# Kernel optimization log

Measured on AMD Instinct MI355X. Metric: run time of the kernel, lower is better.

Reference implementation:

```python
import jax, jax.numpy as jnp
import numpy as np

K = 5          # kernel_size per dim
B = 100        # batch size (hard-coded in source)
GRID = 28
NUM_FIRST_FC = 49  # adjs[2].size(0) = 7*7


def spline_conv(x, edge_index, pseudo, W, root, bias):
    """Degree-1 open B-spline graph conv (SplineGCN).
    x: [N, Cin]; edge_index: [2, E] (src, dst); pseudo: [E, 2] in [0,1];
    W: [K*K, Cin, Cout]; root: [Cin, Cout]; bias: [Cout].
    out_i = mean_{j->i} sum_taps b_tap(u_ij) * (x_j @ W[k_tap]) + x_i @ root + bias
    """
    N = x.shape[0]
    src, dst = edge_index[0], edge_index[1]
    pos = pseudo * (K - 1)                     # open spline: scale to [0, K-1]
    kf = jnp.floor(pos)
    frac = pos - kf                            # [E, 2]
    k0 = kf.astype(jnp.int32)
    k1 = jnp.minimum(k0 + 1, K - 1)
    # Precompute x @ W[k] for all 25 kernel indices: [N, K*K, Cout]
    y = jnp.einsum('ni,kio->nko', x, W)
    fx, fy = frac[:, 0], frac[:, 1]
    taps = [
        (k0[:, 0], k0[:, 1], (1 - fx) * (1 - fy)),
        (k0[:, 0], k1[:, 1], (1 - fx) * fy),
        (k1[:, 0], k0[:, 1], fx * (1 - fy)),
        (k1[:, 0], k1[:, 1], fx * fy),
    ]
    msg = jnp.zeros((src.shape[0], W.shape[2]), dtype=x.dtype)
    for ax, ay, w in taps:
        msg = msg + w[:, None] * y[src, ax * K + ay]   # gather [E, Cout]
    agg = jax.ops.segment_sum(msg, dst, num_segments=N)
    deg = jax.ops.segment_sum(jnp.ones_like(msg[:, 0]), dst, num_segments=N)
    return agg / jnp.maximum(deg, 1.0)[:, None] + x @ root + bias


def max_pool2(x):  # x: [b, H, W, C] -> [b, H/2, W/2, C] (same math as NCHW pool)
    b, h, w, c = x.shape
    return x.reshape(b, h // 2, 2, w // 2, 2, c).max(axis=(2, 4))


def setup_inputs() -> dict:
    key = jax.random.key(0)
    ks = jax.random.split(key, 16)
    N0, N1 = B * GRID * GRID, B * (GRID // 2) * (GRID // 2)
    E0, E1 = N0 * 8, N1 * 8
    s = 0.1
    return {
        'x': jax.random.normal(ks[0], (N0, 1), dtype=jnp.float32),
        'pseudo0': jax.random.uniform(ks[1], (E0, 2), dtype=jnp.float32),
        'pseudo1': jax.random.uniform(ks[2], (E1, 2), dtype=jnp.float32),
        'W1': jax.random.normal(ks[3], (K * K, 1, 32), dtype=jnp.float32) * s,
        'root1': jax.random.normal(ks[4], (1, 32), dtype=jnp.float32) * s,
        'b1': jnp.zeros((32,), dtype=jnp.float32),
        'W2': jax.random.normal(ks[5], (K * K, 32, 64), dtype=jnp.float32) * s,
        'root2': jax.random.normal(ks[6], (32, 64), dtype=jnp.float32) * s,
        'b2': jnp.zeros((64,), dtype=jnp.float32),
        'fc1_w': jax.random.normal(ks[7], (NUM_FIRST_FC * 64, 512), dtype=jnp.float32) * 0.02,
        'fc1_b': jnp.zeros((512,), dtype=jnp.float32),
        'fc2_w': jax.random.normal(ks[8], (512, 10), dtype=jnp.float32) * 0.02,
        'fc2_b': jnp.zeros((10,), dtype=jnp.float32),
        'edge_index0': jax.random.randint(ks[9], (2, E0), 0, N0, dtype=jnp.int32),
        'edge_index1': jax.random.randint(ks[10], (2, E1), 0, N1, dtype=jnp.int32),
    }


def reference(x, pseudo0, pseudo1, W1, root1, b1, W2, root2, b2,
              fc1_w, fc1_b, fc2_w, fc2_b, edge_index0, edge_index1):
    elu = jax.nn.elu
    # conv1 on 28x28 grid graph
    h = elu(spline_conv(x, edge_index0, pseudo0, W1, root1, b1))   # [B*784, 32]
    h = h.reshape(-1, GRID, GRID, 32)                              # [B, 28, 28, 32]
    h = max_pool2(h)                                               # [B, 14, 14, 32]
    h = h.reshape(-1, 32)                                          # [B*196, 32]
    # conv2 on 14x14 grid graph
    h = elu(spline_conv(h, edge_index1, pseudo1, W2, root2, b2))   # [B*196, 64]
    # faithful replication of the source's reshapes: (B*196) rows -> (B/4, 28, 28, 64)
    h = h.reshape(-1, GRID, GRID, 64)                              # [25, 28, 28, 64]
    h = max_pool2(h)                                               # [25, 14, 14, 64]
    h = h.reshape(-1, NUM_FIRST_FC * 64)                           # [100, 3136]
    h = elu(h @ fc1_w + fc1_b)
    # F.dropout with training=False (eval) is identity
    h = elu(h @ fc2_w + fc2_b)
    return jax.nn.log_softmax(h, axis=-1)
```

## Files before the change

kernel.cpp:

```cpp
#include <hip/hip_runtime.h>
#include <hip/hip_bf16.h>

#define KK 5
constexpr int N0 = 78400;
constexpr int E0 = 627200;
constexpr int N1 = 19600;
constexpr int E1 = 156800;
constexpr int C1 = 32, C2 = 64;
constexpr int BSZ = 100;
constexpr int FC1_IN = 3136, FC1_OUT = 512;
constexpr int KEXT = 832;
constexpr int ULS = 836;
constexpr int UBS = 856;
constexpr int KZ = 7;

constexpr int NB0 = 1400;
constexpr int CAP0 = 576;
constexpr int NB1 = 1225;
constexpr int CAP1 = 224;
constexpr int NBT = NB0 + NB1;

constexpr float SC1  = 4194304.f;
constexpr float ISC1 = 1.f / 4194304.f;
constexpr float SC2  = 1048576.f;
constexpr float ISC2 = 1.f / 1048576.f;

typedef __attribute__((ext_vector_type(8))) short bf16x8;
typedef __attribute__((ext_vector_type(4))) float f32x4;

__device__ __forceinline__ unsigned short f2bf(float f) {
    union { float f; unsigned u; } v; v.f = f;
    unsigned u = v.u;
    unsigned r = (u + 0x7FFF + ((u >> 16) & 1)) >> 16;
    return (unsigned short)r;
}
__device__ __forceinline__ float bf2f(unsigned short h) {
    return __uint_as_float(((unsigned)h) << 16);
}

__device__ __forceinline__ unsigned fenc(float f) {
    unsigned u = __float_as_uint(f);
    return (u & 0x80000000u) ? ~u : (u | 0x80000000u);
}
__device__ __forceinline__ unsigned short fdec_bf(unsigned e) {
    unsigned u = (e & 0x80000000u) ? (e & 0x7FFFFFFFu) : ~e;
    return f2bf(__uint_as_float(u));
}

__device__ __forceinline__ void taps4(float px, float py,
                                      int& a00, int& a01, int& a10, int& a11,
                                      float& fx, float& fy) {
    float kfx = floorf(px), kfy = floorf(py);
    fx = px - kfx; fy = py - kfy;
    int k0x = min(max((int)kfx, 0), KK - 1);
    int k0y = min(max((int)kfy, 0), KK - 1);
    int k1x = min(k0x + 1, KK - 1), k1y = min(k0y + 1, KK - 1);
    a00 = k0x * KK + k0y; a01 = k0x * KK + k1y;
    a10 = k1x * KK + k0y; a11 = k1x * KK + k1y;
}

__global__ void coarse_bin(const int* __restrict__ ei0, const int* __restrict__ ei1,
                           const float* __restrict__ ps0, const float* __restrict__ ps1,
                           int* __restrict__ gcur,
                           int2* __restrict__ pk0, int2* __restrict__ pk1,
                           const float* __restrict__ fc1w, const float* __restrict__ W2,
                           const float* __restrict__ root2,
                           unsigned short* __restrict__ wt1,
                           unsigned short* __restrict__ w2t,
                           unsigned* __restrict__ pmax) {
    __shared__ int hist[NBT];
    __shared__ int gbase[NBT];
    __shared__ unsigned short tile[64 * 66];
    int t = threadIdx.x;
    if (blockIdx.x >= 192) {
        int pb = blockIdx.x - 192;
        if (pb >= 400) {
            for (int idx = (pb - 400) * 512 + t; idx < 112 * FC1_IN; idx += 8 * 512)
                pmax[idx] = (idx < 100 * FC1_IN) ? 0x007FFFFFu
                                                 : 0x80000000u;
            return;
        }
        if (pb >= 392) {
            int base = (pb - 392) * 6656;
            for (int i2 = t; i2 < 6656; i2 += 512) {
                int idx = base + i2;
                int o = idx / KEXT, k = idx - o * KEXT;
                float v = (k < 800) ? W2[k * 64 + o] : root2[(k - 800) * 64 + o];
                w2t[idx] = f2bf(v);
            }
            return;
        }
        int k0 = (pb >> 3) * 64, j0 = (pb & 7) * 64;
        int jj = t & 63, ks = t >> 6;
        for (int kk = ks; kk < 64; kk += 8)
            tile[kk * 66 + jj] = f2bf(fc1w[(k0 + kk) * FC1_OUT + j0 + jj]);
        __syncthreads();
        int kk2 = t & 63, js = t >> 6;
        for (int j2 = js; j2 < 64; j2 += 8)
            wt1[(j0 + j2) * FC1_IN + k0 + kk2] = tile[kk2 * 66 + j2];
        return;
    }
    for (int i = t; i < NBT; i += 512) hist[i] = 0;
    __syncthreads();
    int e0b = blockIdx.x * 4096;
    int keys[8], rnk[8], pay0[8], pay1[8];
#pragma unroll
    for (int j = 0; j < 8; j++) {
        int e = e0b + t + j * 512;
        int k = -1, p0 = 0, p1v = 0;
        if (e < E0) {
            int dst = ei0[E0 + e];
            int b = dst / 56, low = dst - b * 56;
            k = b;
            float px = ps0[2 * e] * 4.f, py = ps0[2 * e + 1] * 4.f;
            unsigned ux = min((unsigned)(px * 16384.f + 0.5f), 65535u);
            unsigned uy = min((unsigned)(py * 16384.f + 0.5f), 65535u);
            p0 = ei0[e] | (low << 20); p1v = (int)(ux | (uy << 16));
        } else if (e < E0 + E1) {
            int el = e - E0;
            int dst = ei1[E1 + el];
            k = NB0 + (dst >> 4);
            float px = ps1[2 * el] * 4.f, py = ps1[2 * el + 1] * 4.f;
            unsigned ux = min((unsigned)(px * 16384.f + 0.5f), 65535u);
            unsigned uy = min((unsigned)(py * 16384.f + 0.5f), 65535u);
            p0 = ei1[el] | ((dst & 15) << 20); p1v = (int)(ux | (uy << 16));
        }
        keys[j] = k; pay0[j] = p0; pay1[j] = p1v;
    }
#pragma unroll
    for (int j = 0; j < 8; j++)
        if (keys[j] >= 0) rnk[j] = atomicAdd(&hist[keys[j]], 1);
    __syncthreads();
    for (int i = t; i < NBT; i += 512)
        gbase[i] = hist[i] ? atomicAdd(&gcur[i], hist[i]) : 0;
    __syncthreads();
#pragma unroll
    for (int j = 0; j < 8; j++) {
        if (keys[j] >= 0) {
            int k = keys[j];
            int p = gbase[k] + rnk[j];
            if (k < NB0) {
                if (p < CAP0) pk0[k * CAP0 + p] = make_int2(pay0[j], pay1[j]);
            } else {
                if (p < CAP1) pk1[(k - NB0) * CAP1 + p] = make_int2(pay0[j], pay1[j]);
            }
        }
    }
}

__global__ __launch_bounds__(256, 6)
void conv1_pool(const int2* __restrict__ pk0, const int* __restrict__ cnt0,
                const float* __restrict__ x,
                const float* __restrict__ W1,
                const float* __restrict__ root, const float* __restrict__ bias,
                unsigned short* __restrict__ p1b) {
    __shared__ int   Ui[56 * 26];
    __shared__ float h1t[56 * 32];
    int t = threadIdx.x;
    int bb = blockIdx.x;
    int n0 = bb * 56;
    for (int i = t; i < 56 * 26; i += 256) Ui[i] = 0;
    __syncthreads();
    int cnt = min(cnt0[bb], CAP0);
    const int2* bkt = pk0 + bb * CAP0;
    for (int j = t; j < cnt; j += 256) {
        int2 r = bkt[j];
        int src = r.x & 0xFFFFF, low = (r.x >> 20) & 63;
        float px = (float)((unsigned)r.y & 0xFFFF) * (1.f / 16384.f);
        float py = (float)((unsigned)r.y >> 16) * (1.f / 16384.f);
        int a00, a01, a10, a11; float fx, fy;
        taps4(px, py, a00, a01, a10, a11, fx, fy);
        float xv = x[src];
        float gx = 1.f - fx, gy = 1.f - fy;
        int* row = Ui + low * 26;
        atomicAdd(row + a00, __float2int_rn(gx * gy * xv * SC1));
        atomicAdd(row + a01, __float2int_rn(gx * fy * xv * SC1));
        atomicAdd(row + a10, __float2int_rn(fx * gy * xv * SC1));
        atomicAdd(row + a11, __float2int_rn(fx * fy * xv * SC1));
        atomicAdd(row + 25, 1);
    }
    __syncthreads();
    {
        int o = t & 31, ng = t >> 5;
        float w1c[25];
#pragma unroll
        for (int a = 0; a < 25; a++) w1c[a] = W1[a * C1 + o];
        float ro = root[o], bo = bias[o];
        for (int j2 = 0; j2 < 7; j2++) {
            int nl = ng * 7 + j2;
            int n = n0 + nl;
            float acc = 0.f;
#pragma unroll
            for (int a = 0; a < 25; a++) acc += (float)Ui[nl * 26 + a] * w1c[a];
            float invd = ISC1 / fmaxf((float)Ui[nl * 26 + 25], 1.f);
            float v = acc * invd + x[n] * ro + bo;
            h1t[nl * 32 + o] = v > 0.f ? v : expm1f(v);
        }
    }
    __syncthreads();
    for (int i2 = t; i2 < 448; i2 += 256) {
        int o2 = i2 & 31, pc = i2 >> 5;
        float m0 = h1t[(2 * pc) * 32 + o2],      m1 = h1t[(2 * pc + 1) * 32 + o2];
        float m2 = h1t[(28 + 2 * pc) * 32 + o2], m3 = h1t[(28 + 2 * pc + 1) * 32 + o2];
        p1b[(bb * 14 + pc) * C1 + o2] = f2bf(fmaxf(fmaxf(m0, m1), fmaxf(m2, m3)));
    }
}

__global__ __launch_bounds__(512, 2)
void conv2_fused(const unsigned short* __restrict__ p1b, const int2* __restrict__ pk1,
                 const int* __restrict__ cnt1,
                 const unsigned short* __restrict__ w2t,
                 const float* __restrict__ b2, unsigned* __restrict__ pmax) {
    __shared__ int   Ui[16 * ULS];
    __shared__ int   es[CAP1];
    __shared__ int   et[CAP1];
    __shared__ float efx[CAP1], efy[CAP1];
    __shared__ int   degc[16];
    unsigned short* Ub = (unsigned short*)Ui;
    int t = threadIdx.x;
    int bx = blockIdx.x;
    int nb = bx * 16;
    int i = t & 31;
    int g = t >> 5;
    int* up = Ui + g * ULS;
#pragma unroll
    for (int a = 0; a < 25; a++) up[a * 32 + i] = 0;
    up[800 + i] = __float2int_rn(bf2f(p1b[(nb + g) * C1 + i]) * SC2);
    if (t < 16) degc[t] = 0;
    __syncthreads();
    int cnt = min(cnt1[bx], CAP1);
    for (int j = t; j < cnt; j += 512) {
        int2 r = pk1[bx * CAP1 + j];
        es[j] = r.x;
        float px = (float)((unsigned)r.y & 0xFFFF) * (1.f / 16384.f);
        float py = (float)((unsigned)r.y >> 16) * (1.f / 16384.f);
        int a00, a01, a10, a11; float fx, fy;
        taps4(px, py, a00, a01, a10, a11, fx, fy);
        et[j] = a00 | (a01 << 5) | (a10 << 10) | (a11 << 15);
        efx[j] = fx; efy[j] = fy;
        atomicAdd(&degc[(r.x >> 20) & 15], 1);
    }
    __syncthreads();
    for (int j = g; j < cnt; j += 16) {
        int rx = es[j];
        float xv = bf2f(p1b[(rx & 0xFFFFF) * C1 + i]);
        int* row = Ui + ((rx >> 20) & 15) * ULS;
        int m = et[j];
        float fx = efx[j], fy = efy[j];
        float gx = 1.f - fx, gy = 1.f - fy;
        atomicAdd(row + (m & 31) * 32 + i,         __float2int_rn(gx * gy * xv * SC2));
        atomicAdd(row + ((m >> 5) & 31) * 32 + i,  __float2int_rn(gx * fy * xv * SC2));
        atomicAdd(row + ((m >> 10) & 31) * 32 + i, __float2int_rn(fx * gy * xv * SC2));
        atomicAdd(row + ((m >> 15) & 31) * 32 + i, __float2int_rn(fx * fy * xv * SC2));
    }
    __syncthreads();
    {
        int g2 = t >> 5, i2c = t & 31;
        float invd = 1.f / fmaxf((float)degc[g2], 1.f);
        float stap = ISC2 * invd;
        const int* srcp = Ui + g2 * ULS + i2c * 26;
        float rv[26];
#pragma unroll
        for (int j = 0; j < 26; j++) {
            float v = (float)srcp[j];
            rv[j] = (i2c * 26 + j < 800) ? v * stap : v * ISC2;
        }
        __syncthreads();
        unsigned* dstp = (unsigned*)(Ub + g2 * UBS + i2c * 26);
#pragma unroll
        for (int j = 0; j < 13; j++) {
            unsigned lo = f2bf(rv[2 * j]), hi = f2bf(rv[2 * j + 1]);
            dstp[j] = lo | (hi << 16);
        }
    }
    __syncthreads();
    int wv = t >> 6, lane = t & 63, quad = lane >> 4, lrow = lane & 15;
    if (wv < 4) {
        f32x4 acc = {0.f, 0.f, 0.f, 0.f};
        const unsigned short* bbase = w2t + (wv * 16 + lrow) * KEXT;
        const unsigned short* abase = Ub + lrow * UBS;
#pragma unroll
        for (int kc = 0; kc < 26; kc++) {
            bf16x8 a = *(const bf16x8*)(abase + kc * 32 + quad * 8);
            bf16x8 b = *(const bf16x8*)(bbase + kc * 32 + quad * 8);
            acc = __builtin_amdgcn_mfma_f32_16x16x32_bf16(a, b, acc, 0, 0, 0);
        }
        int o = wv * 16 + lrow;
        float bo = b2[o];
#pragma unroll
        for (int r = 0; r < 4; r++) {
            int node = quad * 4 + r;
            float v = acc[r] + bo;
            v = v > 0.f ? v : expm1f(v);
            int n1 = nb + node;
            int b28 = n1 / 784;
            int rem = n1 - b28 * 784;
            int rr = rem / 28, cc = rem - rr * 28;
            int flat = ((b28 * 14 + (rr >> 1)) * 14 + (cc >> 1)) * 64 + o;
            atomicMax(&pmax[flat], fenc(v));
        }
    }
}

__global__ void gemm_fc1(const unsigned* __restrict__ pmax,
                         const unsigned short* __restrict__ wt1,
                         float* __restrict__ z1p) {
    constexpr int AS = 232;
    __shared__ unsigned short as_[16 * AS];
    int t = threadIdx.x;
    int jt = blockIdx.x, mt = blockIdx.y, kz = blockIdx.z;
    int wv = t >> 6, lane = t & 63, quad = lane >> 4, lrow = lane & 15;
    int m0 = mt * 16;
    int kbase = kz * 448;
    const unsigned short* bbase = wt1 + (jt * 64 + wv * 16 + lrow) * FC1_IN + kbase;
    f32x4 acc = {0.f, 0.f, 0.f, 0.f};
    for (int ch = 0; ch < 2; ch++) {
        __syncthreads();
        for (int slot = t; slot < 448; slot += 256) {
            int r = slot / 28, c = slot - (slot / 28) * 28;
            const unsigned* gp = pmax + (m0 + r) * FC1_IN + kbase + ch * 224 + c * 8;
            uint4 e0 = *(const uint4*)gp;
            uint4 e1 = *(const uint4*)(gp + 4);
            unsigned w0 = (unsigned)fdec_bf(e0.x) | ((unsigned)fdec_bf(e0.y) << 16);
            unsigned w1 = (unsigned)fdec_bf(e0.z) | ((unsigned)fdec_bf(e0.w) << 16);
            unsigned w2 = (unsigned)fdec_bf(e1.x) | ((unsigned)fdec_bf(e1.y) << 16);
            unsigned w3 = (unsigned)fdec_bf(e1.z) | ((unsigned)fdec_bf(e1.w) << 16);
            *(uint4*)(as_ + r * AS + c * 8) = make_uint4(w0, w1, w2, w3);
        }
        __syncthreads();
        const unsigned short* ab = as_ + lrow * AS;
        const unsigned short* bb = bbase + ch * 224;
#pragma unroll
        for (int kk = 0; kk < 7; kk++) {
            bf16x8 a = *(const bf16x8*)(ab + kk * 32 + quad * 8);
            bf16x8 b = *(const bf16x8*)(bb + kk * 32 + quad * 8);
            acc = __builtin_amdgcn_mfma_f32_16x16x32_bf16(a, b, acc, 0, 0, 0);
        }
    }
    int n = jt * 64 + wv * 16 + lrow;
#pragma unroll
    for (int r = 0; r < 4; r++) {
        int m = m0 + quad * 4 + r;
        z1p[kz * (112 * FC1_OUT) + m * FC1_OUT + n] = acc[r];
    }
}

__global__ void fc2_lsm(const float* __restrict__ z1p, const float* __restrict__ fc1b,
                        const float* __restrict__ w, const float* __restrict__ fc2b,
                        float* __restrict__ out) {
    int b = blockIdx.x;
    int t = threadIdx.x;
    int wv = t >> 6;
    int lane = t & 63;
    float acc = 0.f;
#pragma unroll
    for (int m = 0; m < 8; m++) {
        int k = lane * 8 + m;
        float xv = fc1b[k];
#pragma unroll
        for (int p = 0; p < KZ; p++)
            xv += z1p[p * (112 * FC1_OUT) + b * FC1_OUT + k];
        xv = xv > 0.f ? xv : expm1f(xv);
        acc += xv * w[k * 10 + wv];
    }
#pragma unroll
    for (int off = 32; off > 0; off >>= 1) acc += __shfl_down(acc, off);
    __shared__ float zs[10];
    if (lane == 0) {
        float z = acc + fc2b[wv];
        zs[wv] = z > 0.f ? z : expm1f(z);
    }
    __syncthreads();
    if (t < 10) {
        float m = -1e30f;
        for (int jj = 0; jj < 10; jj++) m = fmaxf(m, zs[jj]);
        float s = 0.f;
        for (int jj = 0; jj < 10; jj++) s += expf(zs[jj] - m);
        out[b * 10 + t] = zs[t] - m - logf(s);
    }
}

extern "C" void kernel_launch(void* const* d_in, const int* in_sizes, int n_in,
                              void* d_out, int out_size, void* d_ws, size_t ws_size,
                              hipStream_t stream) {
    const float* x     = (const float*)d_in[0];
    const float* ps0   = (const float*)d_in[1];
    const float* ps1   = (const float*)d_in[2];
    const float* W1    = (const float*)d_in[3];
    const float* root1 = (const float*)d_in[4];
    const float* b1    = (const float*)d_in[5];
    const float* W2    = (const float*)d_in[6];
    const float* root2 = (const float*)d_in[7];
    const float* b2v   = (const float*)d_in[8];
    const float* fc1w  = (const float*)d_in[9];
    const float* fc1b  = (const float*)d_in[10];
    const float* fc2w  = (const float*)d_in[11];
    const float* fc2b  = (const float*)d_in[12];
    const int*   ei0   = (const int*)d_in[13];
    const int*   ei1   = (const int*)d_in[14];

    float* ws = (float*)d_ws;
    int*  gcur = (int*)ws;
    int2* pk0  = (int2*)(ws + 2688);
    int2* pk1  = (int2*)(ws + 1615488);
    unsigned short* p1b = (unsigned short*)(ws + 2164288);
    unsigned* pmax = (unsigned*)(ws + 2477888);
    float* z1p = ws + 2829120;
    unsigned short* w2t = (unsigned short*)(ws + 3230528);
    unsigned short* wt1 = (unsigned short*)(ws + 3257152);

    hipMemsetAsync(gcur, 0, (size_t)NBT * sizeof(int), stream);

    coarse_bin<<<600, 512, 0, stream>>>(ei0, ei1, ps0, ps1, gcur, pk0, pk1,
                                        fc1w, W2, root2, wt1, w2t, pmax);
    conv1_pool<<<NB0, 256, 0, stream>>>(pk0, gcur, x, W1, root1, b1, p1b);
    conv2_fused<<<NB1, 512, 0, stream>>>(p1b, pk1, gcur + NB0, w2t, b2v, pmax);
    gemm_fc1<<<dim3(8, 7, KZ), 256, 0, stream>>>(pmax, wt1, z1p);
    fc2_lsm<<<BSZ, 640, 0, stream>>>(z1p, fc1b, fc2w, fc2b, (float*)d_out);
}
```

Before: 185.2 us.

## Fuse conv1, conv2, fc1 and fc2 into one persistent cooperative kernel

Replaces four separate kernel launches with a single persistent cooperative kernel that loops over the former block indices and separates stages with grid-wide syncs. This removes the launch gaps and tail effects between stages. In exchange, each stage runs with at most 1024 resident blocks of 512 threads, conv1 switches from 256 to 512 threads per work item with idle threads, and the grid barriers themselves add cost. Shared memory is sized for the largest stage, which may lower occupancy for the conv1 phase.

```diff
diff --git a/kernel.cpp b/kernel.cpp
--- a/kernel.cpp
+++ b/kernel.cpp
@@ -1,5 +1,8 @@
 #include <hip/hip_runtime.h>
 #include <hip/hip_bf16.h>
+#include <hip/hip_cooperative_groups.h>
+
+namespace cg = cooperative_groups;
 
 #define KK 5
 constexpr int N0 = 78400;
@@ -148,235 +151,249 @@
     }
 }
 
-__global__ __launch_bounds__(256, 6)
-void conv1_pool(const int2* __restrict__ pk0, const int* __restrict__ cnt0,
-                const float* __restrict__ x,
-                const float* __restrict__ W1,
-                const float* __restrict__ root, const float* __restrict__ bias,
-                unsigned short* __restrict__ p1b) {
-    __shared__ int   Ui[56 * 26];
-    __shared__ float h1t[56 * 32];
+__global__ __launch_bounds__(512)
+void fused_net(const int2* __restrict__ pk0, const int2* __restrict__ pk1,
+               const int* __restrict__ gcur,
+               const float* __restrict__ x, const float* __restrict__ W1,
+               const float* __restrict__ root1, const float* __restrict__ b1,
+               const unsigned short* __restrict__ w2t, const float* __restrict__ b2,
+               const unsigned short* __restrict__ wt1, const float* __restrict__ fc1b,
+               const float* __restrict__ fc2w, const float* __restrict__ fc2b,
+               unsigned short* __restrict__ p1b, unsigned* __restrict__ pmax,
+               float* __restrict__ z1p, float* __restrict__ out) {
+    cg::grid_group grid = cg::this_grid();
+    __shared__ int UiS[16 * ULS];
+    __shared__ int esS[CAP1];
+    __shared__ int etS[CAP1];
+    __shared__ float efxS[CAP1], efyS[CAP1];
+    __shared__ int degc[16];
     int t = threadIdx.x;
-    int bb = blockIdx.x;
-    int n0 = bb * 56;
-    for (int i = t; i < 56 * 26; i += 256) Ui[i] = 0;
-    __syncthreads();
-    int cnt = min(cnt0[bb], CAP0);
-    const int2* bkt = pk0 + bb * CAP0;
-    for (int j = t; j < cnt; j += 256) {
-        int2 r = bkt[j];
-        int src = r.x & 0xFFFFF, low = (r.x >> 20) & 63;
-        float px = (float)((unsigned)r.y & 0xFFFF) * (1.f / 16384.f);
-        float py = (float)((unsigned)r.y >> 16) * (1.f / 16384.f);
-        int a00, a01, a10, a11; float fx, fy;
-        taps4(px, py, a00, a01, a10, a11, fx, fy);
-        float xv = x[src];
-        float gx = 1.f - fx, gy = 1.f - fy;
-        int* row = Ui + low * 26;
-        atomicAdd(row + a00, __float2int_rn(gx * gy * xv * SC1));
-        atomicAdd(row + a01, __float2int_rn(gx * fy * xv * SC1));
-        atomicAdd(row + a10, __float2int_rn(fx * gy * xv * SC1));
-        atomicAdd(row + a11, __float2int_rn(fx * fy * xv * SC1));
-        atomicAdd(row + 25, 1);
-    }
-    __syncthreads();
+    int i = t & 31, g = t >> 5;
+    int wv = t >> 6, lane = t & 63, quad = lane >> 4, lrow = lane & 15;
+
     {
-        int o = t & 31, ng = t >> 5;
-        float w1c[25];
-#pragma unroll
-        for (int a = 0; a < 25; a++) w1c[a] = W1[a * C1 + o];
-        float ro = root[o], bo = bias[o];
-        for (int j2 = 0; j2 < 7; j2++) {
-            int nl = ng * 7 + j2;
-            int n = n0 + nl;
-            float acc = 0.f;
-#pragma unroll
-            for (int a = 0; a < 25; a++) acc += (float)Ui[nl * 26 + a] * w1c[a];
-            float invd = ISC1 / fmaxf((float)Ui[nl * 26 + 25], 1.f);
-            float v = acc * invd + x[n] * ro + bo;
-            h1t[nl * 32 + o] = v > 0.f ? v : expm1f(v);
-        }
-    }
-    __syncthreads();
-    for (int i2 = t; i2 < 448; i2 += 256) {
-        int o2 = i2 & 31, pc = i2 >> 5;
-        float m0 = h1t[(2 * pc) * 32 + o2],      m1 = h1t[(2 * pc + 1) * 32 + o2];
-        float m2 = h1t[(28 + 2 * pc) * 32 + o2], m3 = h1t[(28 + 2 * pc + 1) * 32 + o2];
-        p1b[(bb * 14 + pc) * C1 + o2] = f2bf(fmaxf(fmaxf(m0, m1), fmaxf(m2, m3)));
-    }
-}
-
-__global__ __launch_bounds__(512, 2)
-void conv2_fused(const unsigned short* __restrict__ p1b, const int2* __restrict__ pk1,
-                 const int* __restrict__ cnt1,
-                 const unsigned short* __restrict__ w2t,
-                 const float* __restrict__ b2, unsigned* __restrict__ pmax) {
-    __shared__ int   Ui[16 * ULS];
-    __shared__ int   es[CAP1];
-    __shared__ int   et[CAP1];
-    __shared__ float efx[CAP1], efy[CAP1];
-    __shared__ int   degc[16];
-    unsigned short* Ub = (unsigned short*)Ui;
-    int t = threadIdx.x;
-    int bx = blockIdx.x;
-    int nb = bx * 16;
-    int i = t & 31;
-    int g = t >> 5;
-    int* up = Ui + g * ULS;
-#pragma unroll
-    for (int a = 0; a < 25; a++) up[a * 32 + i] = 0;
-    up[800 + i] = __float2int_rn(bf2f(p1b[(nb + g) * C1 + i]) * SC2);
-    if (t < 16) degc[t] = 0;
-    __syncthreads();
-    int cnt = min(cnt1[bx], CAP1);
-    for (int j = t; j < cnt; j += 512) {
-        int2 r = pk1[bx * CAP1 + j];
-        es[j] = r.x;
-        float px = (float)((unsigned)r.y & 0xFFFF) * (1.f / 16384.f);
-        float py = (float)((unsigned)r.y >> 16) * (1.f / 16384.f);
-        int a00, a01, a10, a11; float fx, fy;
-        taps4(px, py, a00, a01, a10, a11, fx, fy);
-        et[j] = a00 | (a01 << 5) | (a10 << 10) | (a11 << 15);
-        efx[j] = fx; efy[j] = fy;
-        atomicAdd(&degc[(r.x >> 20) & 15], 1);
-    }
-    __syncthreads();
-    for (int j = g; j < cnt; j += 16) {
-        int rx = es[j];
-        float xv = bf2f(p1b[(rx & 0xFFFFF) * C1 + i]);
-        int* row = Ui + ((rx >> 20) & 15) * ULS;
-        int m = et[j];
-        float fx = efx[j], fy = efy[j];
-        float gx = 1.f - fx, gy = 1.f - fy;
-        atomicAdd(row + (m & 31) * 32 + i,         __float2int_rn(gx * gy * xv * SC2));
-        atomicAdd(row + ((m >> 5) & 31) * 32 + i,  __float2int_rn(gx * fy * xv * SC2));
-        atomicAdd(row + ((m >> 10) & 31) * 32 + i, __float2int_rn(fx * gy * xv * SC2));
-        atomicAdd(row + ((m >> 15) & 31) * 32 + i, __float2int_rn(fx * fy * xv * SC2));
-    }
-    __syncthreads();
+        int* Ui = UiS;
+        float* h1t = (float*)(UiS + 56 * 26);
+        for (int bb = blockIdx.x; bb < NB0; bb += gridDim.x) {
+            int n0 = bb * 56;
+            for (int k = t; k < 56 * 26; k += 512) Ui[k] = 0;
+            __syncthreads();
+            int cnt = min(gcur[bb], CAP0);
+            const int2* bkt = pk0 + bb * CAP0;
+            for (int j = t; j < cnt; j += 512) {
+                int2 r = bkt[j];
+                int src = r.x & 0xFFFFF, low = (r.x >> 20) & 63;
+                float px = (float)((unsigned)r.y & 0xFFFF) * (1.f / 16384.f);
+                float py = (float)((unsigned)r.y >> 16) * (1.f / 16384.f);
+                int a00, a01, a10, a11; float fx, fy;
+                taps4(px, py, a00, a01, a10, a11, fx, fy);
+                float xv = x[src];
+                float gx = 1.f - fx, gy = 1.f - fy;
+                int* row = Ui + low * 26;
+                atomicAdd(row + a00, __float2int_rn(gx * gy * xv * SC1));
+                atomicAdd(row + a01, __float2int_rn(gx * fy * xv * SC1));
+                atomicAdd(row + a10, __float2int_rn(fx * gy * xv * SC1));
+                atomicAdd(row + a11, __float2int_rn(fx * fy * xv * SC1));
+                atomicAdd(row + 25, 1);
+            }
+            __syncthreads();
+            {
+                float w1c[25];
+#pragma unroll
+                for (int a = 0; a < 25; a++) w1c[a] = W1[a * C1 + i];
+                float ro = root1[i], bo = b1[i];
+#pragma unroll
+                for (int j2 = 0; j2 < 4; j2++) {
+                    int nl = g * 4 + j2;
+                    if (nl < 56) {
+                        int n = n0 + nl;
+                        float acc = 0.f;
+#pragma unroll
+                        for (int a = 0; a < 25; a++)
+                            acc += (float)Ui[nl * 26 + a] * w1c[a];
+                        float invd = ISC1 / fmaxf((float)Ui[nl * 26 + 25], 1.f);
+                        float v = acc * invd + x[n] * ro + bo;
+                        h1t[nl * 32 + i] = v > 0.f ? v : expm1f(v);
+                    }
+                }
+            }
+            __syncthreads();
+            for (int i2 = t; i2 < 448; i2 += 512) {
+                int o2 = i2 & 31, pc = i2 >> 5;
+                float m0 = h1t[(2 * pc) * 32 + o2],      m1 = h1t[(2 * pc + 1) * 32 + o2];
+                float m2 = h1t[(28 + 2 * pc) * 32 + o2], m3 = h1t[(28 + 2 * pc + 1) * 32 + o2];
+                p1b[(bb * 14 + pc) * C1 + o2] = f2bf(fmaxf(fmaxf(m0, m1), fmaxf(m2, m3)));
+            }
+            __syncthreads();
+        }
+    }
+    grid.sync();
     {
-        int g2 = t >> 5, i2c = t & 31;
-        float invd = 1.f / fmaxf((float)degc[g2], 1.f);
-        float stap = ISC2 * invd;
-        const int* srcp = Ui + g2 * ULS + i2c * 26;
-        float rv[26];
-#pragma unroll
-        for (int j = 0; j < 26; j++) {
-            float v = (float)srcp[j];
-            rv[j] = (i2c * 26 + j < 800) ? v * stap : v * ISC2;
+        unsigned short* Ub = (unsigned short*)UiS;
+        const int* cnt1 = gcur + NB0;
+        for (int bx = blockIdx.x; bx < NB1; bx += gridDim.x) {
+            int nb = bx * 16;
+            int* up = UiS + g * ULS;
+#pragma unroll
+            for (int a = 0; a < 25; a++) up[a * 32 + i] = 0;
+            up[800 + i] = __float2int_rn(bf2f(p1b[(nb + g) * C1 + i]) * SC2);
+            if (t < 16) degc[t] = 0;
+            __syncthreads();
+            int cnt = min(cnt1[bx], CAP1);
+            for (int j = t; j < cnt; j += 512) {
+                int2 r = pk1[bx * CAP1 + j];
+                esS[j] = r.x;
+                float px = (float)((unsigned)r.y & 0xFFFF) * (1.f / 16384.f);
+                float py = (float)((unsigned)r.y >> 16) * (1.f / 16384.f);
+                int a00, a01, a10, a11; float fx, fy;
+                taps4(px, py, a00, a01, a10, a11, fx, fy);
+                etS[j] = a00 | (a01 << 5) | (a10 << 10) | (a11 << 15);
+                efxS[j] = fx; efyS[j] = fy;
+                atomicAdd(&degc[(r.x >> 20) & 15], 1);
+            }
+            __syncthreads();
+            for (int j = g; j < cnt; j += 16) {
+                int rx = esS[j];
+                float xv = bf2f(p1b[(rx & 0xFFFFF) * C1 + i]);
+                int* row = UiS + ((rx >> 20) & 15) * ULS;
+                int m = etS[j];
+                float fx = efxS[j], fy = efyS[j];
+                float gx = 1.f - fx, gy = 1.f - fy;
+                atomicAdd(row + (m & 31) * 32 + i,         __float2int_rn(gx * gy * xv * SC2));
+                atomicAdd(row + ((m >> 5) & 31) * 32 + i,  __float2int_rn(gx * fy * xv * SC2));
+                atomicAdd(row + ((m >> 10) & 31) * 32 + i, __float2int_rn(fx * gy * xv * SC2));
+                atomicAdd(row + ((m >> 15) & 31) * 32 + i, __float2int_rn(fx * fy * xv * SC2));
+            }
+            __syncthreads();
+            {
+                float invd = 1.f / fmaxf((float)degc[g], 1.f);
+                float stap = ISC2 * invd;
+                const int* srcp = UiS + g * ULS + i * 26;
+                float rv[26];
+#pragma unroll
+                for (int j = 0; j < 26; j++) {
+                    float v = (float)srcp[j];
+                    rv[j] = (i * 26 + j < 800) ? v * stap : v * ISC2;
+                }
+                __syncthreads();
+                unsigned* dstp = (unsigned*)(Ub + g * UBS + i * 26);
+#pragma unroll
+                for (int j = 0; j < 13; j++) {
+                    unsigned lo = f2bf(rv[2 * j]), hi = f2bf(rv[2 * j + 1]);
+                    dstp[j] = lo | (hi << 16);
+                }
+            }
+            __syncthreads();
+            if (wv < 4) {
+                f32x4 acc = {0.f, 0.f, 0.f, 0.f};
+                const unsigned short* bbase = w2t + (wv * 16 + lrow) * KEXT;
+                const unsigned short* abase = Ub + lrow * UBS;
+#pragma unroll
+                for (int kc = 0; kc < 26; kc++) {
+                    bf16x8 a = *(const bf16x8*)(abase + kc * 32 + quad * 8);
+                    bf16x8 b = *(const bf16x8*)(bbase + kc * 32 + quad * 8);
+                    acc = __builtin_amdgcn_mfma_f32_16x16x32_bf16(a, b, acc, 0, 0, 0);
+                }
+                int o = wv * 16 + lrow;
+                float bo = b2[o];
+#pragma unroll
+                for (int r = 0; r < 4; r++) {
+                    int node = quad * 4 + r;
+                    float v = acc[r] + bo;
+                    v = v > 0.f ? v : expm1f(v);
+                    int n1 = nb + node;
+                    int b28 = n1 / 784;
+                    int rem = n1 - b28 * 784;
+                    int rr = rem / 28, cc = rem - rr * 28;
+                    int flat = ((b28 * 14 + (rr >> 1)) * 14 + (cc >> 1)) * 64 + o;
+                    atomicMax(&pmax[flat], fenc(v));
+                }
+            }
+            __syncthreads();
+        }
+    }
+    grid.sync();
+    {
+        constexpr int AS = 232;
+        unsigned short* as_ = (unsigned short*)UiS;
+        for (int tau = blockIdx.x; tau < 8 * 7 * KZ; tau += gridDim.x) {
+            int jt = tau & 7, r2 = tau >> 3;
+            int mt = r2 % 7, kz = r2 / 7;
+            int m0 = mt * 16;
+            int kbase = kz * 448;
+            const unsigned short* bbase = wt1 + (jt * 64 + (wv & 3) * 16 + lrow) * FC1_IN + kbase;
+            f32x4 acc = {0.f, 0.f, 0.f, 0.f};
+            for (int ch = 0; ch < 2; ch++) {
+                __syncthreads();
+                for (int slot = t; slot < 448; slot += 512) {
+                    int r = slot / 28, c = slot - (slot / 28) * 28;
+                    const unsigned* gp = pmax + (m0 + r) * FC1_IN + kbase + ch * 224 + c * 8;
+                    uint4 e0 = *(const uint4*)gp;
+                    uint4 e1 = *(const uint4*)(gp + 4);
+                    unsigned w0 = (unsigned)fdec_bf(e0.x) | ((unsigned)fdec_bf(e0.y) << 16);
+                    unsigned w1 = (unsigned)fdec_bf(e0.z) | ((unsigned)fdec_bf(e0.w) << 16);
+                    unsigned w2 = (unsigned)fdec_bf(e1.x) | ((unsigned)fdec_bf(e1.y) << 16);
+                    unsigned w3 = (unsigned)fdec_bf(e1.z) | ((unsigned)fdec_bf(e1.w) << 16);
+                    *(uint4*)(as_ + r * AS + c * 8) = make_uint4(w0, w1, w2, w3);
+                }
+                __syncthreads();
+                if (wv < 4) {
+                    const unsigned short* ab = as_ + lrow * AS;
+                    const unsigned short* bb = bbase + ch * 224;
+#pragma unroll
+                    for (int kk = 0; kk < 7; kk++) {
+                        bf16x8 a = *(const bf16x8*)(ab + kk * 32 + quad * 8);
+                        bf16x8 b = *(const bf16x8*)(bb + kk * 32 + quad * 8);
+                        acc = __builtin_amdgcn_mfma_f32_16x16x32_bf16(a, b, acc, 0, 0, 0);
+                    }
+                }
+            }
+            if (wv < 4) {
+                int n = jt * 64 + wv * 16 + lrow;
+#pragma unroll
+                for (int r = 0; r < 4; r++) {
+                    int m = m0 + quad * 4 + r;
+                    z1p[kz * (112 * FC1_OUT) + m * FC1_OUT + n] = acc[r];
+                }
+            }
+            __syncthreads();
+        }
+    }
+    grid.sync();
+    if (blockIdx.x < BSZ) {
+        int b = blockIdx.x;
+        float* zs = (float*)UiS;
+#pragma unroll
+        for (int rep = 0; rep < 2; rep++) {
+            int cls = wv + rep * 8;
+            if (cls < 10) {
+                float acc = 0.f;
+#pragma unroll
+                for (int m = 0; m < 8; m++) {
+                    int k = lane * 8 + m;
+                    float xv = fc1b[k];
+#pragma unroll
+                    for (int p = 0; p < KZ; p++)
+                        xv += z1p[p * (112 * FC1_OUT) + b * FC1_OUT + k];
+                    xv = xv > 0.f ? xv : expm1f(xv);
+                    acc += xv * fc2w[k * 10 + cls];
+                }
+#pragma unroll
+                for (int off = 32; off > 0; off >>= 1) acc += __shfl_down(acc, off);
+                if (lane == 0) {
+                    float z = acc + fc2b[cls];
+                    zs[cls] = z > 0.f ? z : expm1f(z);
+                }
+            }
         }
         __syncthreads();
-        unsigned* dstp = (unsigned*)(Ub + g2 * UBS + i2c * 26);
-#pragma unroll
-        for (int j = 0; j < 13; j++) {
-            unsigned lo = f2bf(rv[2 * j]), hi = f2bf(rv[2 * j + 1]);
-            dstp[j] = lo | (hi << 16);
-        }
-    }
-    __syncthreads();
-    int wv = t >> 6, lane = t & 63, quad = lane >> 4, lrow = lane & 15;
-    if (wv < 4) {
-        f32x4 acc = {0.f, 0.f, 0.f, 0.f};
-        const unsigned short* bbase = w2t + (wv * 16 + lrow) * KEXT;
-        const unsigned short* abase = Ub + lrow * UBS;
-#pragma unroll
-        for (int kc = 0; kc < 26; kc++) {
-            bf16x8 a = *(const bf16x8*)(abase + kc * 32 + quad * 8);
-            bf16x8 b = *(const bf16x8*)(bbase + kc * 32 + quad * 8);
-            acc = __builtin_amdgcn_mfma_f32_16x16x32_bf16(a, b, acc, 0, 0, 0);
-        }
-        int o = wv * 16 + lrow;
-        float bo = b2[o];
-#pragma unroll
-        for (int r = 0; r < 4; r++) {
-            int node = quad * 4 + r;
-            float v = acc[r] + bo;
-            v = v > 0.f ? v : expm1f(v);
-            int n1 = nb + node;
-            int b28 = n1 / 784;
-            int rem = n1 - b28 * 784;
-            int rr = rem / 28, cc = rem - rr * 28;
-            int flat = ((b28 * 14 + (rr >> 1)) * 14 + (cc >> 1)) * 64 + o;
-            atomicMax(&pmax[flat], fenc(v));
-        }
-    }
-}
-
-__global__ void gemm_fc1(const unsigned* __restrict__ pmax,
-                         const unsigned short* __restrict__ wt1,
-                         float* __restrict__ z1p) {
-    constexpr int AS = 232;
-    __shared__ unsigned short as_[16 * AS];
-    int t = threadIdx.x;
-    int jt = blockIdx.x, mt = blockIdx.y, kz = blockIdx.z;
-    int wv = t >> 6, lane = t & 63, quad = lane >> 4, lrow = lane & 15;
-    int m0 = mt * 16;
-    int kbase = kz * 448;
-    const unsigned short* bbase = wt1 + (jt * 64 + wv * 16 + lrow) * FC1_IN + kbase;
-    f32x4 acc = {0.f, 0.f, 0.f, 0.f};
-    for (int ch = 0; ch < 2; ch++) {
-        __syncthreads();
-        for (int slot = t; slot < 448; slot += 256) {
-            int r = slot / 28, c = slot - (slot / 28) * 28;
-            const unsigned* gp = pmax + (m0 + r) * FC1_IN + kbase + ch * 224 + c * 8;
-            uint4 e0 = *(const uint4*)gp;
-            uint4 e1 = *(const uint4*)(gp + 4);
-            unsigned w0 = (unsigned)fdec_bf(e0.x) | ((unsigned)fdec_bf(e0.y) << 16);
-            unsigned w1 = (unsigned)fdec_bf(e0.z) | ((unsigned)fdec_bf(e0.w) << 16);
-            unsigned w2 = (unsigned)fdec_bf(e1.x) | ((unsigned)fdec_bf(e1.y) << 16);
-            unsigned w3 = (unsigned)fdec_bf(e1.z) | ((unsigned)fdec_bf(e1.w) << 16);
-            *(uint4*)(as_ + r * AS + c * 8) = make_uint4(w0, w1, w2, w3);
-        }
-        __syncthreads();
-        const unsigned short* ab = as_ + lrow * AS;
-        const unsigned short* bb = bbase + ch * 224;
-#pragma unroll
-        for (int kk = 0; kk < 7; kk++) {
-            bf16x8 a = *(const bf16x8*)(ab + kk * 32 + quad * 8);
-            bf16x8 b = *(const bf16x8*)(bb + kk * 32 + quad * 8);
-            acc = __builtin_amdgcn_mfma_f32_16x16x32_bf16(a, b, acc, 0, 0, 0);
-        }
-    }
-    int n = jt * 64 + wv * 16 + lrow;
-#pragma unroll
-    for (int r = 0; r < 4; r++) {
-        int m = m0 + quad * 4 + r;
-        z1p[kz * (112 * FC1_OUT) + m * FC1_OUT + n] = acc[r];
-    }
-}
-
-__global__ void fc2_lsm(const float* __restrict__ z1p, const float* __restrict__ fc1b,
-                        const float* __restrict__ w, const float* __restrict__ fc2b,
-                        float* __restrict__ out) {
-    int b = blockIdx.x;
-    int t = threadIdx.x;
-    int wv = t >> 6;
-    int lane = t & 63;
-    float acc = 0.f;
-#pragma unroll
-    for (int m = 0; m < 8; m++) {
-        int k = lane * 8 + m;
-        float xv = fc1b[k];
-#pragma unroll
-        for (int p = 0; p < KZ; p++)
-            xv += z1p[p * (112 * FC1_OUT) + b * FC1_OUT + k];
-        xv = xv > 0.f ? xv : expm1f(xv);
-        acc += xv * w[k * 10 + wv];
-    }
-#pragma unroll
-    for (int off = 32; off > 0; off >>= 1) acc += __shfl_down(acc, off);
-    __shared__ float zs[10];
-    if (lane == 0) {
-        float z = acc + fc2b[wv];
-        zs[wv] = z > 0.f ? z : expm1f(z);
-    }
-    __syncthreads();
-    if (t < 10) {
-        float m = -1e30f;
-        for (int jj = 0; jj < 10; jj++) m = fmaxf(m, zs[jj]);
-        float s = 0.f;
-        for (int jj = 0; jj < 10; jj++) s += expf(zs[jj] - m);
-        out[b * 10 + t] = zs[t] - m - logf(s);
+        if (t < 10) {
+            float m = -1e30f;
+            for (int jj = 0; jj < 10; jj++) m = fmaxf(m, zs[jj]);
+            float s = 0.f;
+            for (int jj = 0; jj < 10; jj++) s += expf(zs[jj] - m);
+            out[b * 10 + t] = zs[t] - m - logf(s);
+        }
     }
 }
 
@@ -408,13 +425,27 @@
     float* z1p = ws + 2829120;
     unsigned short* w2t = (unsigned short*)(ws + 3230528);
     unsigned short* wt1 = (unsigned short*)(ws + 3257152);
+    float* outp = (float*)d_out;
 
     hipMemsetAsync(gcur, 0, (size_t)NBT * sizeof(int), stream);
 
     coarse_bin<<<600, 512, 0, stream>>>(ei0, ei1, ps0, ps1, gcur, pk0, pk1,
                                         fc1w, W2, root2, wt1, w2t, pmax);
-    conv1_pool<<<NB0, 256, 0, stream>>>(pk0, gcur, x, W1, root1, b1, p1b);
-    conv2_fused<<<NB1, 512, 0, stream>>>(p1b, pk1, gcur + NB0, w2t, b2v, pmax);
-    gemm_fc1<<<dim3(8, 7, KZ), 256, 0, stream>>>(pmax, wt1, z1p);
-    fc2_lsm<<<BSZ, 640, 0, stream>>>(z1p, fc1b, fc2w, fc2b, (float*)d_out);
-}
+
+    static int coopBlocks = 0;
+    if (coopBlocks == 0) {
+        int bpc = 0;
+        hipOccupancyMaxActiveBlocksPerMultiprocessor(&bpc, (const void*)fused_net, 512, 0);
+        if (bpc < 1) bpc = 1;
+        coopBlocks = bpc * 256;
+        if (coopBlocks > 1024) coopBlocks = 1024;
+    }
+    void* args[] = {
+        (void*)&pk0, (void*)&pk1, (void*)&gcur, (void*)&x, (void*)&W1,
+        (void*)&root1, (void*)&b1, (void*)&w2t, (void*)&b2v, (void*)&wt1,
+        (void*)&fc1b, (void*)&fc2w, (void*)&fc2b, (void*)&p1b, (void*)&pmax,
+        (void*)&z1p, (void*)&outp
+    };
+    hipLaunchCooperativeKernel((const void*)fused_net, dim3(coopBlocks), dim3(512),
+                               args, 0, stream);
+}
```

Measured after the change: 303.4 us. +63.8%, slower.

## Bin edges with fewer, larger blocks using two-pass histogram then scatter

Applied to the files above, without the earlier changes.

The edge-binning phase now uses 64 blocks that each cover 12250 edges instead of 192 blocks of 4096. Each block first builds a shared histogram from destination indices alone, reserves global ranges once per bin, then re-reads the edges and scatters them with shared-memory cursor atomics. The aim is fewer global atomics on the bin counters, since each block aggregates more edges per bin. The cost is reading the destination indices twice, running far fewer binning blocks so the GPU is less parallel in this phase, and a nondeterministic order of edges within each bin.

```diff
diff --git a/kernel.cpp b/kernel.cpp
--- a/kernel.cpp
+++ b/kernel.cpp
@@ -20,6 +20,10 @@
 constexpr int CAP1 = 224;
 constexpr int NBT = NB0 + NB1;
 
+constexpr int BIN_BLKS = 64;
+constexpr int EPB = 12250;
+constexpr int EITER = 24;
+
 constexpr float SC1  = 4194304.f;
 constexpr float ISC1 = 1.f / 4194304.f;
 constexpr float SC2  = 1048576.f;
@@ -69,11 +73,11 @@
                            unsigned short* __restrict__ w2t,
                            unsigned* __restrict__ pmax) {
     __shared__ int hist[NBT];
-    __shared__ int gbase[NBT];
+    __shared__ int cur[NBT];
     __shared__ unsigned short tile[64 * 66];
     int t = threadIdx.x;
-    if (blockIdx.x >= 192) {
-        int pb = blockIdx.x - 192;
+    if (blockIdx.x >= BIN_BLKS) {
+        int pb = blockIdx.x - BIN_BLKS;
         if (pb >= 400) {
             for (int idx = (pb - 400) * 512 + t; idx < 112 * FC1_IN; idx += 8 * 512)
                 pmax[idx] = (idx < 100 * FC1_IN) ? 0x007FFFFFu
@@ -102,47 +106,46 @@
     }
     for (int i = t; i < NBT; i += 512) hist[i] = 0;
     __syncthreads();
-    int e0b = blockIdx.x * 4096;
-    int keys[8], rnk[8], pay0[8], pay1[8];
-#pragma unroll
-    for (int j = 0; j < 8; j++) {
-        int e = e0b + t + j * 512;
-        int k = -1, p0 = 0, p1v = 0;
-        if (e < E0) {
-            int dst = ei0[E0 + e];
-            int b = dst / 56, low = dst - b * 56;
-            k = b;
-            float px = ps0[2 * e] * 4.f, py = ps0[2 * e + 1] * 4.f;
-            unsigned ux = min((unsigned)(px * 16384.f + 0.5f), 65535u);
-            unsigned uy = min((unsigned)(py * 16384.f + 0.5f), 65535u);
-            p0 = ei0[e] | (low << 20); p1v = (int)(ux | (uy << 16));
-        } else if (e < E0 + E1) {
-            int el = e - E0;
-            int dst = ei1[E1 + el];
-            k = NB0 + (dst >> 4);
-            float px = ps1[2 * el] * 4.f, py = ps1[2 * el + 1] * 4.f;
-            unsigned ux = min((unsigned)(px * 16384.f + 0.5f), 65535u);
-            unsigned uy = min((unsigned)(py * 16384.f + 0.5f), 65535u);
-            p0 = ei1[el] | ((dst & 15) << 20); p1v = (int)(ux | (uy << 16));
-        }
-        keys[j] = k; pay0[j] = p0; pay1[j] = p1v;
-    }
-#pragma unroll
-    for (int j = 0; j < 8; j++)
-        if (keys[j] >= 0) rnk[j] = atomicAdd(&hist[keys[j]], 1);
+    int ebase = blockIdx.x * EPB;
+    for (int j = 0; j < EITER; j++) {
+        int le = t + j * 512;
+        if (le < EPB) {
+            int e = ebase + le;
+            int k;
+            if (e < E0) k = ei0[E0 + e] / 56;
+            else        k = NB0 + (ei1[E1 + (e - E0)] >> 4);
+            atomicAdd(&hist[k], 1);
+        }
+    }
     __syncthreads();
     for (int i = t; i < NBT; i += 512)
-        gbase[i] = hist[i] ? atomicAdd(&gcur[i], hist[i]) : 0;
-    __syncthreads();
-#pragma unroll
-    for (int j = 0; j < 8; j++) {
-        if (keys[j] >= 0) {
-            int k = keys[j];
-            int p = gbase[k] + rnk[j];
-            if (k < NB0) {
-                if (p < CAP0) pk0[k * CAP0 + p] = make_int2(pay0[j], pay1[j]);
+        cur[i] = hist[i] ? atomicAdd(&gcur[i], hist[i]) : 0;
+    __syncthreads();
+    for (int j = 0; j < EITER; j++) {
+        int le = t + j * 512;
+        if (le < EPB) {
+            int e = ebase + le;
+            if (e < E0) {
+                int dst = ei0[E0 + e];
+                int b = dst / 56, low = dst - b * 56;
+                float px = ps0[2 * e] * 4.f, py = ps0[2 * e + 1] * 4.f;
+                unsigned ux = min((unsigned)(px * 16384.f + 0.5f), 65535u);
+                unsigned uy = min((unsigned)(py * 16384.f + 0.5f), 65535u);
+                int p = atomicAdd(&cur[b], 1);
+                if (p < CAP0)
+                    pk0[b * CAP0 + p] = make_int2(ei0[e] | (low << 20),
+                                                  (int)(ux | (uy << 16)));
             } else {
-                if (p < CAP1) pk1[(k - NB0) * CAP1 + p] = make_int2(pay0[j], pay1[j]);
+                int el = e - E0;
+                int dst = ei1[E1 + el];
+                int b = dst >> 4;
+                float px = ps1[2 * el] * 4.f, py = ps1[2 * el + 1] * 4.f;
+                unsigned ux = min((unsigned)(px * 16384.f + 0.5f), 65535u);
+                unsigned uy = min((unsigned)(py * 16384.f + 0.5f), 65535u);
+                int p = atomicAdd(&cur[NB0 + b], 1);
+                if (p < CAP1)
+                    pk1[b * CAP1 + p] = make_int2(ei1[el] | ((dst & 15) << 20),
+                                                  (int)(ux | (uy << 16)));
             }
         }
     }
@@ -411,8 +414,9 @@
 
     hipMemsetAsync(gcur, 0, (size_t)NBT * sizeof(int), stream);
 
-    coarse_bin<<<600, 512, 0, stream>>>(ei0, ei1, ps0, ps1, gcur, pk0, pk1,
-                                        fc1w, W2, root2, wt1, w2t, pmax);
+    coarse_bin<<<BIN_BLKS + 392 + 8 + 8, 512, 0, stream>>>(
+        ei0, ei1, ps0, ps1, gcur, pk0, pk1,
+        fc1w, W2, root2, wt1, w2t, pmax);
     conv1_pool<<<NB0, 256, 0, stream>>>(pk0, gcur, x, W1, root1, b1, p1b);
     conv2_fused<<<NB1, 512, 0, stream>>>(p1b, pk1, gcur + NB0, w2t, b2v, pmax);
     gemm_fc1<<<dim3(8, 7, KZ), 256, 0, stream>>>(pmax, wt1, z1p);
```

After: 200.7 us. 1.08x slower.
